# Kernel optimization log

Hardware: AMD Instinct MI355X
Metric: run time of the kernel (lower is better)

## Reference

```python
import jax, jax.numpy as jnp
import numpy as np

N_NODES = 50000
N_EDGES = 800000
F_IN, F_HID, F_OUT = 128, 256, 10


def setup_inputs() -> dict:
    key = jax.random.key(0)
    ks = jax.random.split(key, 8)
    x = jax.random.normal(ks[0], (N_NODES, F_IN), dtype=jnp.float32)
    edge_index = jax.random.randint(ks[1], (2, N_EDGES), 0, N_NODES, dtype=jnp.int64)
    # Glorot-ish init for GCNConv weights (PyG GCNConv: lin weight [in,out] + bias [out])
    def glorot(k, fi, fo):
        s = (6.0 / (fi + fo)) ** 0.5
        return jax.random.uniform(k, (fi, fo), minval=-s, maxval=s, dtype=jnp.float32)
    return {
        "x": x,
        "edge_index": edge_index,
        "W1": glorot(ks[2], F_IN, F_HID), "b1": jnp.zeros((F_HID,), jnp.float32),
        "W2": glorot(ks[3], F_HID, F_HID), "b2": jnp.zeros((F_HID,), jnp.float32),
        "W3": glorot(ks[4], F_HID, F_OUT), "b3": jnp.zeros((F_OUT,), jnp.float32),
    }


def _gcn_conv(x, W, b, src, dst, norm, n_nodes):
    # GCNConv: out[dst] += norm_e * (x @ W)[src]; then + bias
    xw = x @ W                                   # [N, F_out]
    msgs = norm[:, None] * xw[src]               # [E+N, F_out] gather
    agg = jax.ops.segment_sum(msgs, dst, num_segments=n_nodes)
    return agg + b


def reference(x, edge_index, W1, b1, W2, b2, W3, b3):
    n = x.shape[0]
    loops = jnp.arange(n, dtype=edge_index.dtype)
    src = jnp.concatenate([edge_index[0], loops])  # source nodes (messages from)
    dst = jnp.concatenate([edge_index[1], loops])  # target nodes (aggregate into)
    # symmetric normalization D^{-1/2} (A+I) D^{-1/2}, degree from target index
    deg = jax.ops.segment_sum(jnp.ones_like(dst, dtype=x.dtype), dst, num_segments=n)
    dinv = jnp.where(deg > 0, jax.lax.rsqrt(deg), 0.0)
    norm = dinv[src] * dinv[dst]

    h = _gcn_conv(x, W1, b1, src, dst, norm, n)
    h = jax.nn.relu(h)                  # dropout is identity in eval mode
    h = _gcn_conv(h, W2, b2, src, dst, norm, n)
    h = jax.nn.relu(h)
    h = _gcn_conv(h, W3, b3, src, dst, norm, n)
    return jax.nn.log_softmax(h, axis=1)
```

## Files before the change

### kernel.cpp

```cpp
#include <hip/hip_runtime.h>
#include <hip/hip_bf16.h>
#include <math.h>

#define F_IN 128
#define F_HID 256
#define F_OUT 10

typedef __attribute__((ext_vector_type(8))) short s16x8;
typedef __attribute__((ext_vector_type(4))) float f32x4;

static __device__ __forceinline__ float b2f(unsigned short u) {
    union { float f; unsigned int u; } c;
    c.u = ((unsigned int)u) << 16;
    return c.f;
}
static __device__ __forceinline__ unsigned short f2b(float f) {
    return __bfloat16_as_ushort(__float2bfloat16(f));
}


__global__ void prep_kernel(const int* __restrict__ dst, int* __restrict__ cnt, int e,
                            const float* __restrict__ x, unsigned short* __restrict__ xb,
                            int xq,
                            const float* __restrict__ W1, unsigned short* __restrict__ W1t,
                            const float* __restrict__ W2, unsigned short* __restrict__ W2t) {
    int i = blockIdx.x * blockDim.x + threadIdx.x;
    int job = blockIdx.y;
    if (job == 0) {
        if (i < e) atomicAdd(&cnt[dst[i]], 1);
    } else if (job == 1) {
        if (i < xq) {
            float4 v = *(const float4*)&x[(size_t)i * 4];
            ushort4 o;
            o.x = f2b(v.x); o.y = f2b(v.y); o.z = f2b(v.z); o.w = f2b(v.w);
            *(ushort4*)&xb[(size_t)i * 4] = o;
        }
    } else if (job == 2) {
        if (i < F_IN * F_HID) {
            int k = i / F_HID, nn = i - k * F_HID;
            W1t[nn * F_IN + k] = f2b(W1[i]);
        }
    } else {
        if (i < F_HID * F_HID) {
            int k = i / F_HID, nn = i - k * F_HID;
            W2t[nn * F_HID + k] = f2b(W2[i]);
        }
    }
}


__global__ void scan1_kernel(const int* __restrict__ cnt, int* __restrict__ rowstart,
                             int* __restrict__ partial, float* __restrict__ dinv, int n) {
    __shared__ int s[256];
    int tid = threadIdx.x;
    int i = blockIdx.x * 256 + tid;
    int v = (i < n) ? cnt[i] : 0;
    s[tid] = v;
    __syncthreads();
    for (int off = 1; off < 256; off <<= 1) {
        int t = (tid >= off) ? s[tid - off] : 0;
        __syncthreads();
        s[tid] += t;
        __syncthreads();
    }
    if (i < n) {
        rowstart[i] = s[tid] - v;
        dinv[i] = rsqrtf((float)(v + 1));
    }
    if (tid == 255) partial[blockIdx.x] = s[255];
}

__global__ void scan2_kernel(int* __restrict__ partial, int nb) {
    __shared__ int s[256];
    int tid = threadIdx.x;
    int v = (tid < nb) ? partial[tid] : 0;
    s[tid] = v;
    __syncthreads();
    for (int off = 1; off < 256; off <<= 1) {
        int t = (tid >= off) ? s[tid - off] : 0;
        __syncthreads();
        s[tid] += t;
        __syncthreads();
    }
    if (tid < nb) partial[tid] = s[tid] - v;
}

__global__ void scan3_kernel(int* __restrict__ rowstart, const int* __restrict__ partial,
                             int n, int e) {
    int i = blockIdx.x * blockDim.x + threadIdx.x;
    if (i < n) rowstart[i] += partial[blockIdx.x];
    if (i == 0) rowstart[n] = e;
}

__global__ void fill_kernel(const int* __restrict__ src, const int* __restrict__ dst,
                            const int* __restrict__ rowstart, int* __restrict__ cursor,
                            const float* __restrict__ dinv, int2* __restrict__ pack, int e) {
    int i = blockIdx.x * blockDim.x + threadIdx.x;
    if (i >= e) return;
    int s = src[i], d = dst[i];
    int pos = rowstart[d] + atomicAdd(&cursor[d], 1);
    float w = dinv[s] * dinv[d];
    pack[pos] = make_int2(s, __float_as_int(w));
}


template <int F>
__global__ __launch_bounds__(256) void agg_kernel(const unsigned short* __restrict__ feat,
                                                  const int* __restrict__ rowstart,
                                                  const int2* __restrict__ pack,
                                                  const float* __restrict__ dinv,
                                                  unsigned short* __restrict__ out, int n) {
    constexpr int LPF = F / 8;
    constexpr int EG = 64 / LPF;
    int wid = threadIdx.x >> 6;
    int lane = threadIdx.x & 63;
    int v = blockIdx.x * 4 + wid;
    if (v >= n) return;
    int eg = lane / LPF;
    int fl = lane % LPF;
    const unsigned short* fp = feat + fl * 8;

    float acc[8];
    {
        float d = dinv[v];
        float sw = (eg == 0) ? d * d : 0.f;
        s16x8 t = *(const s16x8*)&fp[(size_t)v * F];
#pragma unroll
        for (int j = 0; j < 8; ++j) acc[j] = sw * b2f((unsigned short)t[j]);
    }

    int e0 = rowstart[v], e1 = rowstart[v + 1];
    constexpr int STEP = EG * 4;
    int e = e0;
    for (; e + STEP <= e1; e += STEP) {
        int2 p[4];
#pragma unroll
        for (int u = 0; u < 4; ++u) p[u] = pack[e + eg + u * EG];
        s16x8 t[4];
#pragma unroll
        for (int u = 0; u < 4; ++u) t[u] = *(const s16x8*)&fp[(size_t)p[u].x * F];
#pragma unroll
        for (int u = 0; u < 4; ++u) {
            float w = __int_as_float(p[u].y);
#pragma unroll
            for (int j = 0; j < 8; ++j) acc[j] += w * b2f((unsigned short)t[u][j]);
        }
    }
    for (int ee = e + eg; ee < e1; ee += EG) {
        int2 p = pack[ee];
        float w = __int_as_float(p.y);
        s16x8 t = *(const s16x8*)&fp[(size_t)p.x * F];
#pragma unroll
        for (int j = 0; j < 8; ++j) acc[j] += w * b2f((unsigned short)t[j]);
    }

    if (EG == 4) {
#pragma unroll
        for (int j = 0; j < 8; ++j) acc[j] += __shfl_xor(acc[j], 16);
    }
#pragma unroll
    for (int j = 0; j < 8; ++j) acc[j] += __shfl_xor(acc[j], 32);

    if (eg == 0) {
        s16x8 o;
#pragma unroll
        for (int j = 0; j < 8; ++j) o[j] = (short)f2b(acc[j]);
        *(s16x8*)&out[(size_t)v * F + fl * 8] = o;
    }
}


template <int K, bool FUSE3>
__global__ __launch_bounds__(256) void gemm_kernel(const unsigned short* __restrict__ A,
                                                   const unsigned short* __restrict__ Bt,
                                                   const float* __restrict__ bias,
                                                   unsigned short* __restrict__ Cb,
                                                   const float* __restrict__ W3,
                                                   float* __restrict__ hw3, int M) {
    constexpr int N = F_HID;
    __shared__ unsigned short As[64][40];
    __shared__ unsigned short Bs[N][40];
    const int tid = threadIdx.x;
    const int w = tid >> 6, lane = tid & 63;
    const int g = lane >> 4, r16 = lane & 15;
    const int bm = blockIdx.x;

    const int sArow = tid >> 2;
    const int sAkq = (tid & 3) * 8;
    const int garow = bm * 64 + sArow;

    f32x4 acc[16] = {};

    for (int k0 = 0; k0 < K; k0 += 32) {
        uint4 av = make_uint4(0, 0, 0, 0);
        if (garow < M) av = *(const uint4*)&A[(size_t)garow * K + k0 + sAkq];
        uint4 bv0 = *(const uint4*)&Bt[(size_t)tid * K + k0 + 0];
        uint4 bv1 = *(const uint4*)&Bt[(size_t)tid * K + k0 + 8];
        uint4 bv2 = *(const uint4*)&Bt[(size_t)tid * K + k0 + 16];
        uint4 bv3 = *(const uint4*)&Bt[(size_t)tid * K + k0 + 24];
        __syncthreads();
        *(uint4*)&As[sArow][sAkq] = av;
        *(uint4*)&Bs[tid][0] = bv0;
        *(uint4*)&Bs[tid][8] = bv1;
        *(uint4*)&Bs[tid][16] = bv2;
        *(uint4*)&Bs[tid][24] = bv3;
        __syncthreads();

        s16x8 af = *(const s16x8*)&As[w * 16 + r16][g * 8];
#pragma unroll
        for (int cg = 0; cg < 16; ++cg) {
            s16x8 bf = *(const s16x8*)&Bs[cg * 16 + r16][g * 8];
            acc[cg] = __builtin_amdgcn_mfma_f32_16x16x32_bf16(af, bf, acc[cg], 0, 0, 0);
        }
    }

    if constexpr (!FUSE3) {
#pragma unroll
        for (int cg = 0; cg < 16; ++cg) {
            int col = cg * 16 + r16;
            float bs = bias[col];
#pragma unroll
            for (int r = 0; r < 4; ++r) {
                int row = bm * 64 + w * 16 + g * 4 + r;
                if (row < M) {
                    float v = fmaxf(acc[cg][r] + bs, 0.f);
                    Cb[(size_t)row * N + col] = f2b(v);
                }
            }
        }
    } else {
        float* W3s = (float*)&Bs[0][0];
        __syncthreads();
        for (int i = tid; i < N * F_OUT; i += 256) W3s[i] = W3[i];
        __syncthreads();

        float bcol[16];
#pragma unroll
        for (int cg = 0; cg < 16; ++cg) bcol[cg] = bias[cg * 16 + r16];

#pragma unroll
        for (int r = 0; r < 4; ++r) {
            float pj[F_OUT] = {};
#pragma unroll
            for (int cg = 0; cg < 16; ++cg) {
                float v = fmaxf(acc[cg][r] + bcol[cg], 0.f);
                const float* w3r = &W3s[(cg * 16 + r16) * F_OUT];
#pragma unroll
                for (int j = 0; j < F_OUT; ++j) pj[j] += v * w3r[j];
            }
#pragma unroll
            for (int j = 0; j < F_OUT; ++j) {
                pj[j] += __shfl_xor(pj[j], 1);
                pj[j] += __shfl_xor(pj[j], 2);
                pj[j] += __shfl_xor(pj[j], 4);
                pj[j] += __shfl_xor(pj[j], 8);
            }
            if (r16 == 0) {
                int row = bm * 64 + w * 16 + g * 4 + r;
                if (row < M) {
#pragma unroll
                    for (int j = 0; j < F_OUT; ++j) hw3[(size_t)row * F_OUT + j] = pj[j];
                }
            }
        }
    }
}


__global__ void final_kernel(const float* __restrict__ hw3, const int* __restrict__ rowstart,
                             const int2* __restrict__ pack, const float* __restrict__ dinv,
                             const float* __restrict__ b3, float* __restrict__ out, int n) {
    int v = blockIdx.x * blockDim.x + threadIdx.x;
    if (v >= n) return;
    float acc[F_OUT];
    float d = dinv[v];
    float sw = d * d;
#pragma unroll
    for (int j = 0; j < F_OUT; ++j) acc[j] = sw * hw3[(size_t)v * F_OUT + j];
    int e0 = rowstart[v], e1 = rowstart[v + 1];
    for (int e = e0; e < e1; ++e) {
        int2 p = pack[e];
        float w = __int_as_float(p.y);
#pragma unroll
        for (int j = 0; j < F_OUT; ++j) acc[j] += w * hw3[(size_t)p.x * F_OUT + j];
    }
#pragma unroll
    for (int j = 0; j < F_OUT; ++j) acc[j] += b3[j];
    float m = acc[0];
#pragma unroll
    for (int j = 1; j < F_OUT; ++j) m = fmaxf(m, acc[j]);
    float sum = 0.f;
#pragma unroll
    for (int j = 0; j < F_OUT; ++j) sum += expf(acc[j] - m);
    float lse = m + logf(sum);
#pragma unroll
    for (int j = 0; j < F_OUT; ++j) out[(size_t)v * F_OUT + j] = acc[j] - lse;
}


extern "C" void kernel_launch(void* const* d_in, const int* in_sizes, int n_in,
                              void* d_out, int out_size, void* d_ws, size_t ws_size,
                              hipStream_t stream) {
    const float* x  = (const float*)d_in[0];
    const int*   ei = (const int*)d_in[1];
    const float* W1 = (const float*)d_in[2];
    const float* b1 = (const float*)d_in[3];
    const float* W2 = (const float*)d_in[4];
    const float* b2 = (const float*)d_in[5];
    const float* W3 = (const float*)d_in[6];
    const float* b3 = (const float*)d_in[7];
    float* out = (float*)d_out;

    int n = in_sizes[0] / F_IN;
    int e = in_sizes[1] / 2;
    const int* srcp = ei;
    const int* dstp = ei + e;

    size_t off = 0;
    auto alloc = [&](size_t bytes) -> char* {
        char* p = (char*)d_ws + off;
        off += (bytes + 255) & ~(size_t)255;
        return p;
    };
    size_t cntpad = ((size_t)n * 4 + 255) & ~(size_t)255;
    int*   cnt      = (int*)alloc((size_t)n * 4);
    int*   cursor   = (int*)alloc((size_t)n * 4);
    int*   rowstart = (int*)alloc((size_t)(n + 1) * 4);
    int*   partial  = (int*)alloc(1024 * 4);
    int2*  pack     = (int2*)alloc((size_t)e * 8);
    float* dinv     = (float*)alloc((size_t)n * 4);
    unsigned short* xb   = (unsigned short*)alloc((size_t)n * F_IN * 2);
    unsigned short* aggb = (unsigned short*)alloc((size_t)n * F_HID * 2);
    unsigned short* h1b  = (unsigned short*)alloc((size_t)n * F_HID * 2);
    unsigned short* W1t  = (unsigned short*)alloc((size_t)F_IN * F_HID * 2);
    unsigned short* W2t  = (unsigned short*)alloc((size_t)F_HID * F_HID * 2);
    float* hw3 = (float*)alloc((size_t)n * F_OUT * 4);

    const int TB = 256;
    hipMemsetAsync(cnt, 0, cntpad + (size_t)n * 4, stream);

    int xq = (int)((size_t)n * F_IN / 4);
    int prepmax = e > xq ? e : xq;
    dim3 gp((prepmax + TB - 1) / TB, 4);
    prep_kernel<<<gp, TB, 0, stream>>>(dstp, cnt, e, x, xb, xq, W1, W1t, W2, W2t);

    int nb = (n + TB - 1) / TB;
    scan1_kernel<<<nb, TB, 0, stream>>>(cnt, rowstart, partial, dinv, n);
    scan2_kernel<<<1, TB, 0, stream>>>(partial, nb);
    scan3_kernel<<<nb, TB, 0, stream>>>(rowstart, partial, n, e);
    fill_kernel<<<(e + TB - 1) / TB, TB, 0, stream>>>(srcp, dstp, rowstart, cursor, dinv,
                                                      pack, e);

    int nwave = (n + 3) / 4;
    int gblocks = (n + 63) / 64;

    agg_kernel<F_IN><<<nwave, 256, 0, stream>>>(xb, rowstart, pack, dinv, aggb, n);
    gemm_kernel<F_IN, false><<<gblocks, 256, 0, stream>>>(aggb, W1t, b1, h1b, nullptr, nullptr, n);

    agg_kernel<F_HID><<<nwave, 256, 0, stream>>>(h1b, rowstart, pack, dinv, aggb, n);
    gemm_kernel<F_HID, true><<<gblocks, 256, 0, stream>>>(aggb, W2t, b2, nullptr, W3, hw3, n);

    final_kernel<<<(n + 255) / 256, 256, 0, stream>>>(hw3, rowstart, pack, dinv, b3, out, n);
}
```

Baseline: 263.8 us.

## Merge three-kernel scan into one block and read GEMM operands directly

The three scan kernels are replaced by a single 1024-thread block in which each thread serially sums a chunk, the chunk totals are scanned in shared memory, and each thread then writes its chunk's row starts and dinv values. This removes two launches and the partial-sum round trip, but runs the whole scan on a single block. Separately, the GEMM no longer stages A and B through LDS: each wave loads its MFMA fragments straight from global memory, relying on L2 for reuse of the shared weight matrix. This drops the per-iteration barriers and LDS traffic at the cost of more global loads per block.

```diff
diff --git a/kernel.cpp b/kernel.cpp
--- a/kernel.cpp
+++ b/kernel.cpp
@@ -49,47 +49,32 @@
 }
 
 
-__global__ void scan1_kernel(const int* __restrict__ cnt, int* __restrict__ rowstart,
-                             int* __restrict__ partial, float* __restrict__ dinv, int n) {
-    __shared__ int s[256];
+__global__ __launch_bounds__(1024) void scan_kernel(const int* __restrict__ cnt,
+                                                    int* __restrict__ rowstart,
+                                                    float* __restrict__ dinv, int n, int e) {
+    __shared__ int s[1024];
     int tid = threadIdx.x;
-    int i = blockIdx.x * 256 + tid;
-    int v = (i < n) ? cnt[i] : 0;
-    s[tid] = v;
+    int per = (n + 1023) >> 10;
+    int lo = tid * per;
+    int hi = lo + per; if (hi > n) hi = n;
+    int sum = 0;
+    for (int i = lo; i < hi; ++i) sum += cnt[i];
+    s[tid] = sum;
     __syncthreads();
-    for (int off = 1; off < 256; off <<= 1) {
+    for (int off = 1; off < 1024; off <<= 1) {
         int t = (tid >= off) ? s[tid - off] : 0;
         __syncthreads();
         s[tid] += t;
         __syncthreads();
     }
-    if (i < n) {
-        rowstart[i] = s[tid] - v;
-        dinv[i] = rsqrtf((float)(v + 1));
-    }
-    if (tid == 255) partial[blockIdx.x] = s[255];
-}
-
-__global__ void scan2_kernel(int* __restrict__ partial, int nb) {
-    __shared__ int s[256];
-    int tid = threadIdx.x;
-    int v = (tid < nb) ? partial[tid] : 0;
-    s[tid] = v;
-    __syncthreads();
-    for (int off = 1; off < 256; off <<= 1) {
-        int t = (tid >= off) ? s[tid - off] : 0;
-        __syncthreads();
-        s[tid] += t;
-        __syncthreads();
-    }
-    if (tid < nb) partial[tid] = s[tid] - v;
-}
-
-__global__ void scan3_kernel(int* __restrict__ rowstart, const int* __restrict__ partial,
-                             int n, int e) {
-    int i = blockIdx.x * blockDim.x + threadIdx.x;
-    if (i < n) rowstart[i] += partial[blockIdx.x];
-    if (i == 0) rowstart[n] = e;
+    int run = (tid > 0) ? s[tid - 1] : 0;
+    for (int i = lo; i < hi; ++i) {
+        int c = cnt[i];
+        rowstart[i] = run;
+        run += c;
+        dinv[i] = rsqrtf((float)(c + 1));
+    }
+    if (tid == 1023) rowstart[n] = e;
 }
 
 __global__ void fill_kernel(const int* __restrict__ src, const int* __restrict__ dst,
@@ -178,38 +163,29 @@
                                                    const float* __restrict__ W3,
                                                    float* __restrict__ hw3, int M) {
     constexpr int N = F_HID;
-    __shared__ unsigned short As[64][40];
-    __shared__ unsigned short Bs[N][40];
     const int tid = threadIdx.x;
     const int w = tid >> 6, lane = tid & 63;
     const int g = lane >> 4, r16 = lane & 15;
     const int bm = blockIdx.x;
 
-    const int sArow = tid >> 2;
-    const int sAkq = (tid & 3) * 8;
-    const int garow = bm * 64 + sArow;
+    __shared__ float W3s[FUSE3 ? (N * F_OUT) : 1];
+    if constexpr (FUSE3) {
+        for (int i = tid; i < N * F_OUT; i += 256) W3s[i] = W3[i];
+    }
+
+    const int arow = bm * 64 + w * 16 + r16;
+    const bool aok = arow < M;
+    const unsigned short* ap = A + (size_t)arow * K + g * 8;
+    const unsigned short* bp = Bt + (size_t)r16 * K + g * 8;
 
     f32x4 acc[16] = {};
 
     for (int k0 = 0; k0 < K; k0 += 32) {
-        uint4 av = make_uint4(0, 0, 0, 0);
-        if (garow < M) av = *(const uint4*)&A[(size_t)garow * K + k0 + sAkq];
-        uint4 bv0 = *(const uint4*)&Bt[(size_t)tid * K + k0 + 0];
-        uint4 bv1 = *(const uint4*)&Bt[(size_t)tid * K + k0 + 8];
-        uint4 bv2 = *(const uint4*)&Bt[(size_t)tid * K + k0 + 16];
-        uint4 bv3 = *(const uint4*)&Bt[(size_t)tid * K + k0 + 24];
-        __syncthreads();
-        *(uint4*)&As[sArow][sAkq] = av;
-        *(uint4*)&Bs[tid][0] = bv0;
-        *(uint4*)&Bs[tid][8] = bv1;
-        *(uint4*)&Bs[tid][16] = bv2;
-        *(uint4*)&Bs[tid][24] = bv3;
-        __syncthreads();
-
-        s16x8 af = *(const s16x8*)&As[w * 16 + r16][g * 8];
+        s16x8 af = {};
+        if (aok) af = *(const s16x8*)(ap + k0);
 #pragma unroll
         for (int cg = 0; cg < 16; ++cg) {
-            s16x8 bf = *(const s16x8*)&Bs[cg * 16 + r16][g * 8];
+            s16x8 bf = *(const s16x8*)(bp + (size_t)cg * 16 * K + k0);
             acc[cg] = __builtin_amdgcn_mfma_f32_16x16x32_bf16(af, bf, acc[cg], 0, 0, 0);
         }
     }
@@ -229,11 +205,7 @@
             }
         }
     } else {
-        float* W3s = (float*)&Bs[0][0];
         __syncthreads();
-        for (int i = tid; i < N * F_OUT; i += 256) W3s[i] = W3[i];
-        __syncthreads();
-
         float bcol[16];
 #pragma unroll
         for (int cg = 0; cg < 16; ++cg) bcol[cg] = bias[cg * 16 + r16];
@@ -326,7 +298,6 @@
     int*   cnt      = (int*)alloc((size_t)n * 4);
     int*   cursor   = (int*)alloc((size_t)n * 4);
     int*   rowstart = (int*)alloc((size_t)(n + 1) * 4);
-    int*   partial  = (int*)alloc(1024 * 4);
     int2*  pack     = (int2*)alloc((size_t)e * 8);
     float* dinv     = (float*)alloc((size_t)n * 4);
     unsigned short* xb   = (unsigned short*)alloc((size_t)n * F_IN * 2);
@@ -344,10 +315,7 @@
     dim3 gp((prepmax + TB - 1) / TB, 4);
     prep_kernel<<<gp, TB, 0, stream>>>(dstp, cnt, e, x, xb, xq, W1, W1t, W2, W2t);
 
-    int nb = (n + TB - 1) / TB;
-    scan1_kernel<<<nb, TB, 0, stream>>>(cnt, rowstart, partial, dinv, n);
-    scan2_kernel<<<1, TB, 0, stream>>>(partial, nb);
-    scan3_kernel<<<nb, TB, 0, stream>>>(rowstart, partial, n, e);
+    scan_kernel<<<1, 1024, 0, stream>>>(cnt, rowstart, dinv, n, e);
     fill_kernel<<<(e + TB - 1) / TB, TB, 0, stream>>>(srcp, dstp, rowstart, cursor, dinv,
                                                       pack, e);
 
```

Result: slower. 426.8 us (+61.8%).

## Fuse neighbor aggregation into GEMM via shared-memory A tile; merge scan kernels

Applied to the files above, without the earlier changes.

Each GEMM block now aggregates its own 64 rows of neighbor features directly into shared memory, then runs the MFMA GEMM from that tile. This removes the intermediate aggregated-feature buffer write and read, and two kernel launches per layer. The second and third scan kernels are also merged, with every block redoing the small partial-sum scan. In exchange, each wave now processes 16 nodes serially, so only 782 blocks run the gather phase instead of 12.5k. That may lower memory-level parallelism during the gather, and the larger shared-memory tile may reduce occupancy.

```diff
diff --git a/kernel.cpp b/kernel.cpp
--- a/kernel.cpp
+++ b/kernel.cpp
@@ -70,7 +70,8 @@
     if (tid == 255) partial[blockIdx.x] = s[255];
 }
 
-__global__ void scan2_kernel(int* __restrict__ partial, int nb) {
+__global__ void scan3_kernel(int* __restrict__ rowstart, const int* __restrict__ partial,
+                             int nb, int n, int e) {
     __shared__ int s[256];
     int tid = threadIdx.x;
     int v = (tid < nb) ? partial[tid] : 0;
@@ -82,13 +83,10 @@
         s[tid] += t;
         __syncthreads();
     }
-    if (tid < nb) partial[tid] = s[tid] - v;
-}
-
-__global__ void scan3_kernel(int* __restrict__ rowstart, const int* __restrict__ partial,
-                             int n, int e) {
-    int i = blockIdx.x * blockDim.x + threadIdx.x;
-    if (i < n) rowstart[i] += partial[blockIdx.x];
+    int boff = (blockIdx.x > 0) ? s[blockIdx.x - 1] : 0;
+    __syncthreads();
+    int i = blockIdx.x * 256 + tid;
+    if (i < n) rowstart[i] += boff;
     if (i == 0) rowstart[n] = e;
 }
 
@@ -104,109 +102,98 @@
 }
 
 
-template <int F>
-__global__ __launch_bounds__(256) void agg_kernel(const unsigned short* __restrict__ feat,
-                                                  const int* __restrict__ rowstart,
-                                                  const int2* __restrict__ pack,
-                                                  const float* __restrict__ dinv,
-                                                  unsigned short* __restrict__ out, int n) {
-    constexpr int LPF = F / 8;
-    constexpr int EG = 64 / LPF;
-    int wid = threadIdx.x >> 6;
-    int lane = threadIdx.x & 63;
-    int v = blockIdx.x * 4 + wid;
-    if (v >= n) return;
-    int eg = lane / LPF;
-    int fl = lane % LPF;
-    const unsigned short* fp = feat + fl * 8;
-
-    float acc[8];
-    {
-        float d = dinv[v];
-        float sw = (eg == 0) ? d * d : 0.f;
-        s16x8 t = *(const s16x8*)&fp[(size_t)v * F];
-#pragma unroll
-        for (int j = 0; j < 8; ++j) acc[j] = sw * b2f((unsigned short)t[j]);
-    }
-
-    int e0 = rowstart[v], e1 = rowstart[v + 1];
-    constexpr int STEP = EG * 4;
-    int e = e0;
-    for (; e + STEP <= e1; e += STEP) {
-        int2 p[4];
-#pragma unroll
-        for (int u = 0; u < 4; ++u) p[u] = pack[e + eg + u * EG];
-        s16x8 t[4];
-#pragma unroll
-        for (int u = 0; u < 4; ++u) t[u] = *(const s16x8*)&fp[(size_t)p[u].x * F];
-#pragma unroll
-        for (int u = 0; u < 4; ++u) {
-            float w = __int_as_float(p[u].y);
-#pragma unroll
-            for (int j = 0; j < 8; ++j) acc[j] += w * b2f((unsigned short)t[u][j]);
-        }
-    }
-    for (int ee = e + eg; ee < e1; ee += EG) {
-        int2 p = pack[ee];
-        float w = __int_as_float(p.y);
-        s16x8 t = *(const s16x8*)&fp[(size_t)p.x * F];
-#pragma unroll
-        for (int j = 0; j < 8; ++j) acc[j] += w * b2f((unsigned short)t[j]);
-    }
-
-    if (EG == 4) {
-#pragma unroll
-        for (int j = 0; j < 8; ++j) acc[j] += __shfl_xor(acc[j], 16);
-    }
-#pragma unroll
-    for (int j = 0; j < 8; ++j) acc[j] += __shfl_xor(acc[j], 32);
-
-    if (eg == 0) {
-        s16x8 o;
-#pragma unroll
-        for (int j = 0; j < 8; ++j) o[j] = (short)f2b(acc[j]);
-        *(s16x8*)&out[(size_t)v * F + fl * 8] = o;
-    }
-}
-
-
 template <int K, bool FUSE3>
-__global__ __launch_bounds__(256) void gemm_kernel(const unsigned short* __restrict__ A,
-                                                   const unsigned short* __restrict__ Bt,
-                                                   const float* __restrict__ bias,
-                                                   unsigned short* __restrict__ Cb,
-                                                   const float* __restrict__ W3,
-                                                   float* __restrict__ hw3, int M) {
+__global__ __launch_bounds__(256) void fused_kernel(const unsigned short* __restrict__ feat,
+                                                    const int* __restrict__ rowstart,
+                                                    const int2* __restrict__ pack,
+                                                    const float* __restrict__ dinv,
+                                                    const unsigned short* __restrict__ Bt,
+                                                    const float* __restrict__ bias,
+                                                    unsigned short* __restrict__ Cb,
+                                                    const float* __restrict__ W3,
+                                                    float* __restrict__ hw3, int M) {
     constexpr int N = F_HID;
-    __shared__ unsigned short As[64][40];
+    constexpr int KP = K + 8;
+    __shared__ unsigned short As[64][KP];
     __shared__ unsigned short Bs[N][40];
     const int tid = threadIdx.x;
     const int w = tid >> 6, lane = tid & 63;
     const int g = lane >> 4, r16 = lane & 15;
     const int bm = blockIdx.x;
 
-    const int sArow = tid >> 2;
-    const int sAkq = (tid & 3) * 8;
-    const int garow = bm * 64 + sArow;
+    {
+        constexpr int LPF = K / 8;
+        constexpr int EG = 64 / LPF;
+        constexpr int STEP = EG * 4;
+        const int eg = lane / LPF;
+        const int fl = lane % LPF;
+        const unsigned short* fp = feat + fl * 8;
+
+        for (int i = 0; i < 16; ++i) {
+            int v = bm * 64 + w * 16 + i;
+            if (v >= M) break;
+            float acc[8];
+            {
+                float d = dinv[v];
+                float sw = (eg == 0) ? d * d : 0.f;
+                s16x8 t = *(const s16x8*)&fp[(size_t)v * K];
+#pragma unroll
+                for (int j = 0; j < 8; ++j) acc[j] = sw * b2f((unsigned short)t[j]);
+            }
+            int e0 = rowstart[v], e1 = rowstart[v + 1];
+            int e = e0;
+            for (; e + STEP <= e1; e += STEP) {
+                int2 p[4];
+#pragma unroll
+                for (int u = 0; u < 4; ++u) p[u] = pack[e + eg + u * EG];
+                s16x8 t[4];
+#pragma unroll
+                for (int u = 0; u < 4; ++u) t[u] = *(const s16x8*)&fp[(size_t)p[u].x * K];
+#pragma unroll
+                for (int u = 0; u < 4; ++u) {
+                    float wv = __int_as_float(p[u].y);
+#pragma unroll
+                    for (int j = 0; j < 8; ++j) acc[j] += wv * b2f((unsigned short)t[u][j]);
+                }
+            }
+            for (int ee = e + eg; ee < e1; ee += EG) {
+                int2 p = pack[ee];
+                float wv = __int_as_float(p.y);
+                s16x8 t = *(const s16x8*)&fp[(size_t)p.x * K];
+#pragma unroll
+                for (int j = 0; j < 8; ++j) acc[j] += wv * b2f((unsigned short)t[j]);
+            }
+            if (EG == 4) {
+#pragma unroll
+                for (int j = 0; j < 8; ++j) acc[j] += __shfl_xor(acc[j], 16);
+            }
+#pragma unroll
+            for (int j = 0; j < 8; ++j) acc[j] += __shfl_xor(acc[j], 32);
+            if (eg == 0) {
+                s16x8 o;
+#pragma unroll
+                for (int j = 0; j < 8; ++j) o[j] = (short)f2b(acc[j]);
+                *(s16x8*)&As[w * 16 + i][fl * 8] = o;
+            }
+        }
+    }
+    __syncthreads();
 
     f32x4 acc[16] = {};
 
     for (int k0 = 0; k0 < K; k0 += 32) {
-        uint4 av = make_uint4(0, 0, 0, 0);
-        if (garow < M) av = *(const uint4*)&A[(size_t)garow * K + k0 + sAkq];
         uint4 bv0 = *(const uint4*)&Bt[(size_t)tid * K + k0 + 0];
         uint4 bv1 = *(const uint4*)&Bt[(size_t)tid * K + k0 + 8];
         uint4 bv2 = *(const uint4*)&Bt[(size_t)tid * K + k0 + 16];
         uint4 bv3 = *(const uint4*)&Bt[(size_t)tid * K + k0 + 24];
-        __syncthreads();
-        *(uint4*)&As[sArow][sAkq] = av;
+        if (k0) __syncthreads();
         *(uint4*)&Bs[tid][0] = bv0;
         *(uint4*)&Bs[tid][8] = bv1;
         *(uint4*)&Bs[tid][16] = bv2;
         *(uint4*)&Bs[tid][24] = bv3;
         __syncthreads();
 
-        s16x8 af = *(const s16x8*)&As[w * 16 + r16][g * 8];
+        s16x8 af = *(const s16x8*)&As[w * 16 + r16][k0 + g * 8];
 #pragma unroll
         for (int cg = 0; cg < 16; ++cg) {
             s16x8 bf = *(const s16x8*)&Bs[cg * 16 + r16][g * 8];
@@ -329,11 +316,10 @@
     int*   partial  = (int*)alloc(1024 * 4);
     int2*  pack     = (int2*)alloc((size_t)e * 8);
     float* dinv     = (float*)alloc((size_t)n * 4);
-    unsigned short* xb   = (unsigned short*)alloc((size_t)n * F_IN * 2);
-    unsigned short* aggb = (unsigned short*)alloc((size_t)n * F_HID * 2);
-    unsigned short* h1b  = (unsigned short*)alloc((size_t)n * F_HID * 2);
-    unsigned short* W1t  = (unsigned short*)alloc((size_t)F_IN * F_HID * 2);
-    unsigned short* W2t  = (unsigned short*)alloc((size_t)F_HID * F_HID * 2);
+    unsigned short* xb  = (unsigned short*)alloc((size_t)n * F_IN * 2);
+    unsigned short* h1b = (unsigned short*)alloc((size_t)n * F_HID * 2);
+    unsigned short* W1t = (unsigned short*)alloc((size_t)F_IN * F_HID * 2);
+    unsigned short* W2t = (unsigned short*)alloc((size_t)F_HID * F_HID * 2);
     float* hw3 = (float*)alloc((size_t)n * F_OUT * 4);
 
     const int TB = 256;
@@ -346,19 +332,17 @@
 
     int nb = (n + TB - 1) / TB;
     scan1_kernel<<<nb, TB, 0, stream>>>(cnt, rowstart, partial, dinv, n);
-    scan2_kernel<<<1, TB, 0, stream>>>(partial, nb);
-    scan3_kernel<<<nb, TB, 0, stream>>>(rowstart, partial, n, e);
+    scan3_kernel<<<nb, TB, 0, stream>>>(rowstart, partial, nb, n, e);
     fill_kernel<<<(e + TB - 1) / TB, TB, 0, stream>>>(srcp, dstp, rowstart, cursor, dinv,
                                                       pack, e);
 
-    int nwave = (n + 3) / 4;
     int gblocks = (n + 63) / 64;
 
-    agg_kernel<F_IN><<<nwave, 256, 0, stream>>>(xb, rowstart, pack, dinv, aggb, n);
-    gemm_kernel<F_IN, false><<<gblocks, 256, 0, stream>>>(aggb, W1t, b1, h1b, nullptr, nullptr, n);
-
-    agg_kernel<F_HID><<<nwave, 256, 0, stream>>>(h1b, rowstart, pack, dinv, aggb, n);
-    gemm_kernel<F_HID, true><<<gblocks, 256, 0, stream>>>(aggb, W2t, b2, nullptr, W3, hw3, n);
+    fused_kernel<F_IN, false><<<gblocks, 256, 0, stream>>>(xb, rowstart, pack, dinv,
+                                                           W1t, b1, h1b, nullptr, nullptr, n);
+
+    fused_kernel<F_HID, true><<<gblocks, 256, 0, stream>>>(h1b, rowstart, pack, dinv,
+                                                           W2t, b2, nullptr, W3, hw3, n);
 
     final_kernel<<<(n + 255) / 256, 256, 0, stream>>>(hw3, rowstart, pack, dinv, b3, out, n);
 }
```

Result: slower. 362.5 us (+37.4%).
